# Performance work log

Hardware: AMD Instinct MI355X
Metric: run time of the kernel (lower is better)

Reference implementation:

```python
import jax, jax.numpy as jnp
import numpy as np

BN_EPS = 1e-3  # TF batch_norm default epsilon


def _three_nn(xyz1, xyz2):
    # xyz1: [B,N,3], xyz2: [B,M,3] -> squared dists [B,N,3], idx [B,N,3]
    d = (jnp.sum(xyz1 * xyz1, -1)[:, :, None]
         - 2.0 * jnp.einsum('bnd,bmd->bnm', xyz1, xyz2)
         + jnp.sum(xyz2 * xyz2, -1)[:, None, :])  # [B,N,M]
    neg, idx = jax.lax.top_k(-d, 3)
    return -neg, idx


def _conv_bn(x, W, b, g, beta, act):
    # 1x1 conv == dense over channel dim; BN over batch+point axes (B,N)
    y = jnp.einsum('bnc,cd->bnd', x, W) + b
    mu = jnp.mean(y, axis=(0, 1))
    var = jnp.var(y, axis=(0, 1))
    y = (y - mu) * jax.lax.rsqrt(var + BN_EPS) * g + beta
    return jax.nn.relu(y) if act else y


def setup_inputs() -> dict:
    key = jax.random.key(0)
    ks = jax.random.split(key, 6)
    B, N, M, C1, C2 = 16, 4096, 1024, 128, 256
    xyz1 = jax.random.normal(ks[0], (B, N, 3), jnp.float32)
    xyz2 = jax.random.normal(ks[1], (B, M, 3), jnp.float32)
    points1 = jax.random.normal(ks[2], (B, N, C1), jnp.float32)
    points2 = jax.random.normal(ks[3], (B, M, C2), jnp.float32)
    Cin = C1 + C2
    W0 = jax.random.normal(ks[4], (Cin, 256), jnp.float32) * (1.0 / np.sqrt(Cin))
    W1 = jax.random.normal(ks[5], (256, 128), jnp.float32) * (1.0 / np.sqrt(256))
    return {
        'xyz1': xyz1, 'points1': points1, 'xyz2': xyz2, 'points2': points2,
        'W0': W0, 'b0': jnp.zeros((256,), jnp.float32),
        'g0': jnp.ones((256,), jnp.float32), 'be0': jnp.zeros((256,), jnp.float32),
        'W1': W1, 'b1': jnp.zeros((128,), jnp.float32),
        'g1': jnp.ones((128,), jnp.float32), 'be1': jnp.zeros((128,), jnp.float32),
    }


def reference(xyz1, points1, xyz2, points2, W0, b0, g0, be0, W1, b1, g1, be1):
    dist, idx = _three_nn(xyz1, xyz2)            # [B,N,3]
    dist = jnp.maximum(dist, 1e-10)
    w = 1.0 / dist
    w = w / jnp.sum(w, axis=2, keepdims=True)    # [B,N,3]
    B = points2.shape[0]
    bidx = jnp.arange(B)[:, None, None]
    nbr = points2[bidx, idx]                     # [B,N,3,C2] gather
    interp = jnp.einsum('bnk,bnkc->bnc', w, nbr)
    x = jnp.concatenate([interp, points1], axis=2)  # [B,N,C1+C2]
    x = _conv_bn(x, W0, b0, g0, be0, act=True)
    x = _conv_bn(x, W1, b1, g1, be1, act=True)   # last_mlp_activation=True
    return x
```

## Files before the change

### kernel.cpp

```cpp
#include <hip/hip_runtime.h>
#include <hip/hip_bf16.h>
#include <stdint.h>

typedef __attribute__((ext_vector_type(4))) float f32x4;
typedef __attribute__((ext_vector_type(2))) float f32x2;
typedef __attribute__((ext_vector_type(8))) __bf16 bf16x8;

__device__ __forceinline__ unsigned short f2bf(float f) {
  unsigned u = __float_as_uint(f);
  unsigned r = (u + 0x7fffu + ((u >> 16) & 1u)) >> 16;
  return (unsigned short)r;
}
__device__ __forceinline__ float bf2f(unsigned short h) {
  return __uint_as_float(((unsigned)h) << 16);
}

__device__ __forceinline__ void load_lds16(const void* g, void* l) {
  __builtin_amdgcn_global_load_lds(
      (const __attribute__((address_space(1))) unsigned int*)g,
      (__attribute__((address_space(3))) unsigned int*)l, 16, 0, 0);
}

__device__ __forceinline__ void vwait(int n) {
  switch (n) {
    case 8: asm volatile("s_waitcnt vmcnt(8)" ::: "memory"); break;
    case 6: asm volatile("s_waitcnt vmcnt(6)" ::: "memory"); break;
    case 4: asm volatile("s_waitcnt vmcnt(4)" ::: "memory"); break;
    case 3: asm volatile("s_waitcnt vmcnt(3)" ::: "memory"); break;
    default: asm volatile("s_waitcnt vmcnt(0)" ::: "memory"); break;
  }
  __builtin_amdgcn_sched_barrier(0);
}

__global__ __launch_bounds__(256) void prep_kernel(
    const float* __restrict__ W0, const float* __restrict__ W1,
    const float* __restrict__ P2f, unsigned short* __restrict__ W0t,
    unsigned short* __restrict__ W1t, unsigned short* __restrict__ P2,
    float* __restrict__ stats) {
  int id = blockIdx.x * 256 + threadIdx.x;
  if (blockIdx.x == 0) {
    for (int i = threadIdx.x; i < 1536; i += 256) stats[i] = 0.f;
  }
  if (id < 256 * 384) {
    int n = id / 384, k = id - n * 384;
    W0t[id] = f2bf(W0[k * 256 + n]);
  }
  if (id < 128 * 256) {
    int n = id / 256, k = id - n * 256;
    W1t[id] = f2bf(W1[k * 128 + n]);
  }
  if (id < 1048576) {
    f32x4 v = ((const f32x4*)P2f)[id];
    ushort4 o = make_ushort4(f2bf(v[0]), f2bf(v[1]), f2bf(v[2]), f2bf(v[3]));
    ((ushort4*)P2)[id] = o;
  }
}

__global__ __launch_bounds__(256) void three_nn_kernel(
    const float* __restrict__ xyz1, const float* __restrict__ xyz2,
    float* __restrict__ W3, int* __restrict__ I3) {
  __shared__ __align__(16) float sx[1024];
  __shared__ __align__(16) float sy[1024];
  __shared__ __align__(16) float sz[1024];
  __shared__ __align__(16) float sn[1024];
  const int b = blockIdx.y;
  const int n0 = blockIdx.x * 32;
  const int tid = threadIdx.x;

  const float* xb = xyz2 + (size_t)b * 3072;
  for (int i = tid; i < 1024; i += 256) {
    float x = xb[i * 3 + 0], y = xb[i * 3 + 1], z = xb[i * 3 + 2];
    sx[i] = x; sy[i] = y; sz[i] = z;
    sn[i] = x * x + y * y + z * z;
  }
  __syncthreads();

  const int pt = tid >> 3, q = tid & 7;
  const int n = n0 + pt;
  const float* p = xyz1 + ((size_t)b * 4096 + n) * 3;
  const float px = p[0], py = p[1], pz = p[2];
  const float cx = -2.f * px, cy = -2.f * py, cz = -2.f * pz;

  float d0 = 3e38f, d1 = 3e38f, d2 = 3e38f;
  int i0 = 0, i1 = 0, i2 = 0;
  auto ins = [&](float e, int j) {
    const bool c0 = e < d0, c1 = e < d1, c2 = e < d2;
    const float nd2 = c1 ? d1 : (c2 ? e : d2);
    const int   ni2 = c1 ? i1 : (c2 ? j : i2);
    const float nd1 = c0 ? d0 : (c1 ? e : d1);
    const int   ni1 = c0 ? i0 : (c1 ? j : i1);
    d0 = c0 ? e : d0; i0 = c0 ? j : i0;
    d1 = nd1; i1 = ni1;
    d2 = nd2; i2 = ni2;
  };

  const f32x4* vx = (const f32x4*)sx;
  const f32x4* vy = (const f32x4*)sy;
  const f32x4* vz = (const f32x4*)sz;
  const f32x4* vn = (const f32x4*)sn;
  for (int jj = 0; jj < 32; jj++) {
    const int c = jj * 8 + q;
    f32x4 ax = vx[c], ay = vy[c], az = vz[c], an = vn[c];
#pragma unroll
    for (int u = 0; u < 4; u++) {
      float d = fmaf(ax[u], cx, fmaf(ay[u], cy, fmaf(az[u], cz, an[u])));
      ins(d, c * 4 + u);
    }
  }
#pragma unroll
  for (int off = 1; off <= 4; off <<= 1) {
    float e0 = __shfl_xor(d0, off, 64);
    float e1 = __shfl_xor(d1, off, 64);
    float e2 = __shfl_xor(d2, off, 64);
    int j0 = __shfl_xor(i0, off, 64);
    int j1 = __shfl_xor(i1, off, 64);
    int j2 = __shfl_xor(i2, off, 64);
    ins(e0, j0); ins(e1, j1); ins(e2, j2);
  }

  if (q == 0) {
    const float pn = fmaf(px, px, fmaf(py, py, pz * pz));
    float t0 = fmaxf(d0 + pn, 1e-10f);
    float t1 = fmaxf(d1 + pn, 1e-10f);
    float t2 = fmaxf(d2 + pn, 1e-10f);
    float w0 = 1.f / t0, w1 = 1.f / t1, w2 = 1.f / t2;
    float inv = 1.f / (w0 + w1 + w2);
    const int row = b * 4096 + n;
    W3[row * 3 + 0] = w0 * inv;
    W3[row * 3 + 1] = w1 * inv;
    W3[row * 3 + 2] = w2 * inv;
    I3[row * 3 + 0] = (b << 10) + i0;
    I3[row * 3 + 1] = (b << 10) + i1;
    I3[row * 3 + 2] = (b << 10) + i2;
  }
}

__global__ __launch_bounds__(256) void interp_concat_kernel(
    const float* __restrict__ points1, const unsigned short* __restrict__ P2,
    const float* __restrict__ W3, const int* __restrict__ I3,
    unsigned short* __restrict__ X) {
  const int gw = blockIdx.x * 4 + (threadIdx.x >> 6);
  const int lane = threadIdx.x & 63;
#pragma unroll 2
  for (int pp = 0; pp < 8; pp++) {
    const int row = gw * 8 + pp;
    const float w0 = W3[row * 3 + 0], w1 = W3[row * 3 + 1], w2 = W3[row * 3 + 2];
    const int g0 = I3[row * 3 + 0], g1 = I3[row * 3 + 1], g2 = I3[row * 3 + 2];
    const ushort4 a0 = *(const ushort4*)(P2 + (size_t)g0 * 256 + lane * 4);
    const ushort4 a1 = *(const ushort4*)(P2 + (size_t)g1 * 256 + lane * 4);
    const ushort4 a2 = *(const ushort4*)(P2 + (size_t)g2 * 256 + lane * 4);
    float o0 = bf2f(a0.x) * w0 + bf2f(a1.x) * w1 + bf2f(a2.x) * w2;
    float o1 = bf2f(a0.y) * w0 + bf2f(a1.y) * w1 + bf2f(a2.y) * w2;
    float o2 = bf2f(a0.z) * w0 + bf2f(a1.z) * w1 + bf2f(a2.z) * w2;
    float o3 = bf2f(a0.w) * w0 + bf2f(a1.w) * w1 + bf2f(a2.w) * w2;
    unsigned int lo = (unsigned)f2bf(o0) | ((unsigned)f2bf(o1) << 16);
    unsigned int hi = (unsigned)f2bf(o2) | ((unsigned)f2bf(o3) << 16);
    *(uint2*)(X + (size_t)row * 384 + lane * 4) = make_uint2(lo, hi);
    const f32x2 qv = ((const f32x2*)(points1 + (size_t)row * 128))[lane];
    unsigned int pq = (unsigned)f2bf(qv.x) | ((unsigned)f2bf(qv.y) << 16);
    *(unsigned int*)(X + (size_t)row * 384 + 256 + lane * 2) = pq;
  }
}

__global__ __launch_bounds__(512) void gemm1_kernel(
    const unsigned short* __restrict__ A, const unsigned short* __restrict__ Bt,
    const float* __restrict__ bvec, unsigned short* __restrict__ Y,
    float* __restrict__ ssum, float* __restrict__ ssq) {
  __shared__ __align__(16) char smem[131072];
  unsigned short* S = (unsigned short*)smem;
  const int m0 = blockIdx.x * 256;
  const int tid = threadIdx.x;
  const int wv = tid >> 6, lane = tid & 63;
  const int wm = wv >> 2, wn = wv & 3;
  f32x4 acc[8][4] = {};

  auto stage = [&](int t) {
    const int k0 = t * 32;
    unsigned short* Ab = S + (t & 3) * 16384;
    unsigned short* Bb = Ab + 8192;
#pragma unroll
    for (int i = 0; i < 2; i++) {
      const int c = (wv * 2 + i) * 64 + lane;
      const int row = c >> 2, kp = c & 3;
      const int gk = (kp ^ (row & 3)) * 8;
      load_lds16(A + (size_t)(m0 + row) * 384 + k0 + gk, Ab + (wv * 2 + i) * 512);
      load_lds16(Bt + (size_t)row * 384 + k0 + gk, Bb + (wv * 2 + i) * 512);
    }
  };

  stage(0); stage(1); stage(2);
  for (int t = 0; t < 12; ++t) {
    const int w = 11 - t;
    vwait(w >= 2 ? 8 : w * 4);
    __builtin_amdgcn_s_barrier();
    __builtin_amdgcn_sched_barrier(0);
    if (t < 9) stage(t + 3);
    const unsigned short* Ab = S + (t & 3) * 16384;
    const unsigned short* Bb = Ab + 8192;
    const int q = lane >> 4;
    bf16x8 af[8], bfr[4];
#pragma unroll
    for (int mf = 0; mf < 8; mf++) {
      const int r = wm * 128 + mf * 16 + (lane & 15);
      af[mf] = *(const bf16x8*)(Ab + r * 32 + (q ^ (r & 3)) * 8);
    }
#pragma unroll
    for (int nf = 0; nf < 4; nf++) {
      const int c = wn * 64 + nf * 16 + (lane & 15);
      bfr[nf] = *(const bf16x8*)(Bb + c * 32 + (q ^ (c & 3)) * 8);
    }
    __builtin_amdgcn_s_setprio(1);
#pragma unroll
    for (int mf = 0; mf < 8; mf++)
#pragma unroll
      for (int nf = 0; nf < 4; nf++)
        acc[mf][nf] = __builtin_amdgcn_mfma_f32_16x16x32_bf16(
            af[mf], bfr[nf], acc[mf][nf], 0, 0, 0);
    __builtin_amdgcn_s_setprio(0);
  }
  __syncthreads();

  float s[4] = {0, 0, 0, 0}, s2[4] = {0, 0, 0, 0};
  unsigned short* ep = S + wv * 8192;
#pragma unroll
  for (int mf = 0; mf < 8; mf++) {
#pragma unroll
    for (int nf = 0; nf < 4; nf++) {
      const float bv = bvec[wn * 64 + nf * 16 + (lane & 15)];
      f32x4 v = acc[mf][nf];
#pragma unroll
      for (int r = 0; r < 4; r++) {
        float y = v[r] + bv;
        s[nf] += y;
        s2[nf] += y * y;
        ep[(mf * 16 + (lane >> 4) * 4 + r) * 64 + nf * 16 + (lane & 15)] =
            f2bf(y);
      }
    }
  }
#pragma unroll
  for (int it = 0; it < 16; it++) {
    const int rr = it * 8 + (lane >> 3);
    *(uint4*)(Y + (size_t)(m0 + wm * 128 + rr) * 256 + wn * 64 + (lane & 7) * 8) =
        *(const uint4*)(ep + rr * 64 + (lane & 7) * 8);
  }

#pragma unroll
  for (int nf = 0; nf < 4; nf++) {
    s[nf] += __shfl_xor(s[nf], 16, 64);
    s[nf] += __shfl_xor(s[nf], 32, 64);
    s2[nf] += __shfl_xor(s2[nf], 16, 64);
    s2[nf] += __shfl_xor(s2[nf], 32, 64);
  }
  if (lane < 16) {
#pragma unroll
    for (int nf = 0; nf < 4; nf++) {
      const int col = wn * 64 + nf * 16 + lane;
      atomicAdd(&ssum[col], s[nf]);
      atomicAdd(&ssq[col], s2[nf]);
    }
  }
}

__device__ __forceinline__ uint4 bnpack8(bf16x8 r, f32x4 s0, f32x4 s1,
                                         f32x4 c0, f32x4 c1) {
  unsigned short o[8];
#pragma unroll
  for (int j = 0; j < 8; j++) {
    const float sj = j < 4 ? s0[j] : s1[j - 4];
    const float cj = j < 4 ? c0[j] : c1[j - 4];
    o[j] = f2bf(fmaxf(0.f, fmaf((float)r[j], sj, cj)));
  }
  return make_uint4((unsigned)o[0] | ((unsigned)o[1] << 16),
                    (unsigned)o[2] | ((unsigned)o[3] << 16),
                    (unsigned)o[4] | ((unsigned)o[5] << 16),
                    (unsigned)o[6] | ((unsigned)o[7] << 16));
}

__global__ __launch_bounds__(512) void gemm2_kernel(
    const unsigned short* __restrict__ Yin, const unsigned short* __restrict__ Bt,
    const float* __restrict__ sum1, const float* __restrict__ sq1,
    const float* __restrict__ g0, const float* __restrict__ be0,
    const float* __restrict__ bvec, unsigned short* __restrict__ Y2,
    float* __restrict__ ssum, float* __restrict__ ssq) {
  __shared__ __align__(16) char smem[100352];
  unsigned short* S = (unsigned short*)smem;
  float* scL = (float*)(smem + 98304);
  float* biL = scL + 256;
  const int m0 = blockIdx.x * 256;
  const int tid = threadIdx.x;
  const int wv = tid >> 6, lane = tid & 63;
  const int wm = wv >> 2, wn = wv & 3;
  f32x4 acc[8][2] = {};

  if (tid < 256) {
    const float invN = 1.0f / 65536.0f;
    float mu = sum1[tid] * invN;
    float var = sq1[tid] * invN - mu * mu;
    float sc = g0[tid] * rsqrtf(var + 1e-3f);
    scL[tid] = sc;
    biL[tid] = be0[tid] - mu * sc;
  }
  __syncthreads();

  bf16x8 arg[3][2];
  auto stageT = [&](int t, bf16x8(&ar)[2]) {
    const int k0 = t * 32;
#pragma unroll
    for (int j = 0; j < 2; j++) {
      const int c = tid + j * 512;
      const int row = c >> 2, kp = c & 3;
      const int gk = (kp ^ (row & 3)) * 8;
      ar[j] = *(const bf16x8*)(Yin + (size_t)(m0 + row) * 256 + k0 + gk);
    }
    const int cb = wv * 64 + lane;
    const int rowb = cb >> 2, kpb = cb & 3;
    const int gkb = (kpb ^ (rowb & 3)) * 8;
    load_lds16(Bt + (size_t)rowb * 256 + k0 + gkb,
               S + (t & 3) * 12288 + 8192 + wv * 512);
  };

  stageT(0, arg[0]); stageT(1, arg[1]); stageT(2, arg[2]);
#pragma unroll
  for (int t = 0; t < 8; ++t) {
    const int w = 7 - t;
    vwait(w >= 2 ? 6 : w * 3);
    unsigned short* Ab = S + (t & 3) * 12288;
#pragma unroll
    for (int j = 0; j < 2; j++) {
      const int c = tid + j * 512;
      const int row = c >> 2, kp = c & 3;
      const int gk = (kp ^ (row & 3)) * 8;
      const int kch = t * 32 + gk;
      const f32x4 sA = *(const f32x4*)(scL + kch);
      const f32x4 sB = *(const f32x4*)(scL + kch + 4);
      const f32x4 cA = *(const f32x4*)(biL + kch);
      const f32x4 cB = *(const f32x4*)(biL + kch + 4);
      *(uint4*)(Ab + c * 8) = bnpack8(arg[t % 3][j], sA, sB, cA, cB);
    }
    asm volatile("s_waitcnt lgkmcnt(0)" ::: "memory");
    __builtin_amdgcn_sched_barrier(0);
    __builtin_amdgcn_s_barrier();
    __builtin_amdgcn_sched_barrier(0);
    if (t < 5) stageT(t + 3, arg[t % 3]);
    const unsigned short* Bb = S + (t & 3) * 12288 + 8192;
    const int q = lane >> 4;
    bf16x8 af[8], bfr[2];
#pragma unroll
    for (int mf = 0; mf < 8; mf++) {
      const int r = wm * 128 + mf * 16 + (lane & 15);
      af[mf] = *(const bf16x8*)(Ab + r * 32 + (q ^ (r & 3)) * 8);
    }
#pragma unroll
    for (int nf = 0; nf < 2; nf++) {
      const int c = wn * 32 + nf * 16 + (lane & 15);
      bfr[nf] = *(const bf16x8*)(Bb + c * 32 + (q ^ (c & 3)) * 8);
    }
    __builtin_amdgcn_s_setprio(1);
#pragma unroll
    for (int mf = 0; mf < 8; mf++)
#pragma unroll
      for (int nf = 0; nf < 2; nf++)
        acc[mf][nf] = __builtin_amdgcn_mfma_f32_16x16x32_bf16(
            af[mf], bfr[nf], acc[mf][nf], 0, 0, 0);
    __builtin_amdgcn_s_setprio(0);
  }
  __syncthreads();

  float s[2] = {0, 0}, s2[2] = {0, 0};
  unsigned short* ep = S + wv * 4096;
#pragma unroll
  for (int mf = 0; mf < 8; mf++) {
#pragma unroll
    for (int nf = 0; nf < 2; nf++) {
      const float bv = bvec[wn * 32 + nf * 16 + (lane & 15)];
      f32x4 v = acc[mf][nf];
#pragma unroll
      for (int r = 0; r < 4; r++) {
        float y = v[r] + bv;
        s[nf] += y;
        s2[nf] += y * y;
        ep[(mf * 16 + (lane >> 4) * 4 + r) * 32 + nf * 16 + (lane & 15)] =
            f2bf(y);
      }
    }
  }
#pragma unroll
  for (int it = 0; it < 8; it++) {
    const int rr = it * 16 + (lane >> 2);
    *(uint4*)(Y2 + (size_t)(m0 + wm * 128 + rr) * 128 + wn * 32 + (lane & 3) * 8) =
        *(const uint4*)(ep + rr * 32 + (lane & 3) * 8);
  }

#pragma unroll
  for (int nf = 0; nf < 2; nf++) {
    s[nf] += __shfl_xor(s[nf], 16, 64);
    s[nf] += __shfl_xor(s[nf], 32, 64);
    s2[nf] += __shfl_xor(s2[nf], 16, 64);
    s2[nf] += __shfl_xor(s2[nf], 32, 64);
  }
  if (lane < 16) {
#pragma unroll
    for (int nf = 0; nf < 2; nf++) {
      const int col = wn * 32 + nf * 16 + lane;
      atomicAdd(&ssum[col], s[nf]);
      atomicAdd(&ssq[col], s2[nf]);
    }
  }
}

__global__ __launch_bounds__(256) void bnrelu_out_kernel(
    const unsigned short* __restrict__ Y2, const float* __restrict__ ssum,
    const float* __restrict__ ssq, const float* __restrict__ g,
    const float* __restrict__ be, float* __restrict__ out) {
  __shared__ __align__(16) float scL[128];
  __shared__ __align__(16) float biL[128];
  const int tid = threadIdx.x;
  if (tid < 128) {
    const float invN = 1.0f / 65536.0f;
    float mu = ssum[tid] * invN;
    float var = ssq[tid] * invN - mu * mu;
    float sc = g[tid] * rsqrtf(var + 1e-3f);
    scL[tid] = sc;
    biL[tid] = be[tid] - mu * sc;
  }
  __syncthreads();

  const size_t i = ((size_t)blockIdx.x * 256 + tid) * 8;
  const int c0 = (int)(i & 127);
  uint4 v = *(const uint4*)(Y2 + i);
  const f32x4 sA = *(const f32x4*)(scL + c0);
  const f32x4 sB = *(const f32x4*)(scL + c0 + 4);
  const f32x4 bA = *(const f32x4*)(biL + c0);
  const f32x4 bB = *(const f32x4*)(biL + c0 + 4);
  unsigned int w[4] = {v.x, v.y, v.z, v.w};
  f32x4 o0, o1;
#pragma unroll
  for (int q = 0; q < 2; q++) {
    o0[q * 2 + 0] = fmaxf(0.f, fmaf(bf2f((unsigned short)(w[q] & 0xffff)), sA[q * 2 + 0], bA[q * 2 + 0]));
    o0[q * 2 + 1] = fmaxf(0.f, fmaf(bf2f((unsigned short)(w[q] >> 16)),   sA[q * 2 + 1], bA[q * 2 + 1]));
    o1[q * 2 + 0] = fmaxf(0.f, fmaf(bf2f((unsigned short)(w[q + 2] & 0xffff)), sB[q * 2 + 0], bB[q * 2 + 0]));
    o1[q * 2 + 1] = fmaxf(0.f, fmaf(bf2f((unsigned short)(w[q + 2] >> 16)),   sB[q * 2 + 1], bB[q * 2 + 1]));
  }
  *(f32x4*)(out + i) = o0;
  *(f32x4*)(out + i + 4) = o1;
}

extern "C" void kernel_launch(void* const* d_in, const int* in_sizes, int n_in,
                              void* d_out, int out_size, void* d_ws,
                              size_t ws_size, hipStream_t stream) {
  const float* xyz1 = (const float*)d_in[0];
  const float* points1 = (const float*)d_in[1];
  const float* xyz2 = (const float*)d_in[2];
  const float* points2 = (const float*)d_in[3];
  const float* W0 = (const float*)d_in[4];
  const float* b0 = (const float*)d_in[5];
  const float* g0 = (const float*)d_in[6];
  const float* be0 = (const float*)d_in[7];
  const float* W1 = (const float*)d_in[8];
  const float* b1 = (const float*)d_in[9];
  const float* g1 = (const float*)d_in[10];
  const float* be1 = (const float*)d_in[11];

  char* ws = (char*)d_ws;
  unsigned short* X = (unsigned short*)(ws);
  unsigned short* Y2 = (unsigned short*)(ws);
  unsigned short* Y = (unsigned short*)(ws + 50331648);
  unsigned short* P2 = (unsigned short*)(ws + 50331648);
  float* W3 = (float*)(ws + 50331648 + 8388608);
  int* I3 = (int*)(ws + 50331648 + 8388608 + 786432);
  unsigned short* W0t = (unsigned short*)(ws + 83886080);
  unsigned short* W1t = (unsigned short*)(ws + 84082688);
  float* stats = (float*)(ws + 84148224);
  float* sum1 = stats, *sq1 = stats + 256;
  float* sum2 = stats + 1024, *sq2 = stats + 1152;
  float* outF = (float*)d_out;

  prep_kernel<<<4096, 256, 0, stream>>>(W0, W1, points2, W0t, W1t, P2, stats);
  three_nn_kernel<<<dim3(128, 16), 256, 0, stream>>>(xyz1, xyz2, W3, I3);
  interp_concat_kernel<<<2048, 256, 0, stream>>>(points1, P2, W3, I3, X);
  gemm1_kernel<<<256, 512, 0, stream>>>(X, W0t, b0, Y, sum1, sq1);
  gemm2_kernel<<<256, 512, 0, stream>>>(Y, W1t, sum1, sq1, g0, be0, b1, Y2,
                                        sum2, sq2);
  bnrelu_out_kernel<<<4096, 256, 0, stream>>>(Y2, sum2, sq2, g1, be1, outF);
}
```

Measured before the change: 132.6 us.

## Merge prep into three-NN launch and double gemm1 block to 16 waves

Fuses the bf16 conversion/prep kernel into the three-NN kernel as extra blocks of one launch, removing a kernel launch and letting the memory-bound prep overlap with the compute-bound nearest-neighbour search. Gemm1 now uses 1024 threads per block (16 waves, each owning a 64x64 sub-tile) instead of 8 waves with 128x64 tiles. This halves per-wave accumulator registers and the per-thread staging loads, with adjusted vmcnt waits. The trade-off is less MFMA reuse per LDS fragment load and more waves contending at each barrier.

```diff
diff --git a/kernel.cpp b/kernel.cpp
--- a/kernel.cpp
+++ b/kernel.cpp
@@ -27,45 +27,49 @@
     case 6: asm volatile("s_waitcnt vmcnt(6)" ::: "memory"); break;
     case 4: asm volatile("s_waitcnt vmcnt(4)" ::: "memory"); break;
     case 3: asm volatile("s_waitcnt vmcnt(3)" ::: "memory"); break;
+    case 2: asm volatile("s_waitcnt vmcnt(2)" ::: "memory"); break;
     default: asm volatile("s_waitcnt vmcnt(0)" ::: "memory"); break;
   }
   __builtin_amdgcn_sched_barrier(0);
 }
 
-__global__ __launch_bounds__(256) void prep_kernel(
+__global__ __launch_bounds__(256) void nn_prep_kernel(
+    const float* __restrict__ xyz1, const float* __restrict__ xyz2,
     const float* __restrict__ W0, const float* __restrict__ W1,
-    const float* __restrict__ P2f, unsigned short* __restrict__ W0t,
+    const float* __restrict__ P2f, float* __restrict__ W3,
+    int* __restrict__ I3, unsigned short* __restrict__ W0t,
     unsigned short* __restrict__ W1t, unsigned short* __restrict__ P2,
     float* __restrict__ stats) {
-  int id = blockIdx.x * 256 + threadIdx.x;
-  if (blockIdx.x == 0) {
-    for (int i = threadIdx.x; i < 1536; i += 256) stats[i] = 0.f;
-  }
-  if (id < 256 * 384) {
-    int n = id / 384, k = id - n * 384;
-    W0t[id] = f2bf(W0[k * 256 + n]);
-  }
-  if (id < 128 * 256) {
-    int n = id / 256, k = id - n * 256;
-    W1t[id] = f2bf(W1[k * 128 + n]);
-  }
-  if (id < 1048576) {
-    f32x4 v = ((const f32x4*)P2f)[id];
-    ushort4 o = make_ushort4(f2bf(v[0]), f2bf(v[1]), f2bf(v[2]), f2bf(v[3]));
-    ((ushort4*)P2)[id] = o;
-  }
-}
-
-__global__ __launch_bounds__(256) void three_nn_kernel(
-    const float* __restrict__ xyz1, const float* __restrict__ xyz2,
-    float* __restrict__ W3, int* __restrict__ I3) {
+  const int bid = blockIdx.x;
+  const int tid = threadIdx.x;
+  if (bid >= 2048) {
+    const int pid = bid - 2048;
+    const int id = pid * 256 + tid;
+    if (pid == 0) {
+      for (int i = tid; i < 1536; i += 256) stats[i] = 0.f;
+    }
+    if (id < 256 * 384) {
+      int n = id / 384, k = id - n * 384;
+      W0t[id] = f2bf(W0[k * 256 + n]);
+    }
+    if (id < 128 * 256) {
+      int n = id / 256, k = id - n * 256;
+      W1t[id] = f2bf(W1[k * 128 + n]);
+    }
+    if (id < 1048576) {
+      f32x4 v = ((const f32x4*)P2f)[id];
+      ushort4 o = make_ushort4(f2bf(v[0]), f2bf(v[1]), f2bf(v[2]), f2bf(v[3]));
+      ((ushort4*)P2)[id] = o;
+    }
+    return;
+  }
+
   __shared__ __align__(16) float sx[1024];
   __shared__ __align__(16) float sy[1024];
   __shared__ __align__(16) float sz[1024];
   __shared__ __align__(16) float sn[1024];
-  const int b = blockIdx.y;
-  const int n0 = blockIdx.x * 32;
-  const int tid = threadIdx.x;
+  const int b = bid >> 7;
+  const int n0 = (bid & 127) * 32;
 
   const float* xb = xyz2 + (size_t)b * 3072;
   for (int i = tid; i < 1024; i += 256) {
@@ -162,7 +166,7 @@
   }
 }
 
-__global__ __launch_bounds__(512) void gemm1_kernel(
+__global__ __launch_bounds__(1024) void gemm1_kernel(
     const unsigned short* __restrict__ A, const unsigned short* __restrict__ Bt,
     const float* __restrict__ bvec, unsigned short* __restrict__ Y,
     float* __restrict__ ssum, float* __restrict__ ssq) {
@@ -172,36 +176,32 @@
   const int tid = threadIdx.x;
   const int wv = tid >> 6, lane = tid & 63;
   const int wm = wv >> 2, wn = wv & 3;
-  f32x4 acc[8][4] = {};
+  f32x4 acc[4][4] = {};
 
   auto stage = [&](int t) {
     const int k0 = t * 32;
     unsigned short* Ab = S + (t & 3) * 16384;
     unsigned short* Bb = Ab + 8192;
-#pragma unroll
-    for (int i = 0; i < 2; i++) {
-      const int c = (wv * 2 + i) * 64 + lane;
-      const int row = c >> 2, kp = c & 3;
-      const int gk = (kp ^ (row & 3)) * 8;
-      load_lds16(A + (size_t)(m0 + row) * 384 + k0 + gk, Ab + (wv * 2 + i) * 512);
-      load_lds16(Bt + (size_t)row * 384 + k0 + gk, Bb + (wv * 2 + i) * 512);
-    }
+    const int row = tid >> 2, kp = tid & 3;
+    const int gk = (kp ^ (row & 3)) * 8;
+    load_lds16(A + (size_t)(m0 + row) * 384 + k0 + gk, Ab + wv * 512);
+    load_lds16(Bt + (size_t)row * 384 + k0 + gk, Bb + wv * 512);
   };
 
   stage(0); stage(1); stage(2);
   for (int t = 0; t < 12; ++t) {
     const int w = 11 - t;
-    vwait(w >= 2 ? 8 : w * 4);
+    vwait(w >= 2 ? 4 : w * 2);
     __builtin_amdgcn_s_barrier();
     __builtin_amdgcn_sched_barrier(0);
     if (t < 9) stage(t + 3);
     const unsigned short* Ab = S + (t & 3) * 16384;
     const unsigned short* Bb = Ab + 8192;
     const int q = lane >> 4;
-    bf16x8 af[8], bfr[4];
-#pragma unroll
-    for (int mf = 0; mf < 8; mf++) {
-      const int r = wm * 128 + mf * 16 + (lane & 15);
+    bf16x8 af[4], bfr[4];
+#pragma unroll
+    for (int mf = 0; mf < 4; mf++) {
+      const int r = wm * 64 + mf * 16 + (lane & 15);
       af[mf] = *(const bf16x8*)(Ab + r * 32 + (q ^ (r & 3)) * 8);
     }
 #pragma unroll
@@ -211,7 +211,7 @@
     }
     __builtin_amdgcn_s_setprio(1);
 #pragma unroll
-    for (int mf = 0; mf < 8; mf++)
+    for (int mf = 0; mf < 4; mf++)
 #pragma unroll
       for (int nf = 0; nf < 4; nf++)
         acc[mf][nf] = __builtin_amdgcn_mfma_f32_16x16x32_bf16(
@@ -221,9 +221,9 @@
   __syncthreads();
 
   float s[4] = {0, 0, 0, 0}, s2[4] = {0, 0, 0, 0};
-  unsigned short* ep = S + wv * 8192;
-#pragma unroll
-  for (int mf = 0; mf < 8; mf++) {
+  unsigned short* ep = S + wv * 4096;
+#pragma unroll
+  for (int mf = 0; mf < 4; mf++) {
 #pragma unroll
     for (int nf = 0; nf < 4; nf++) {
       const float bv = bvec[wn * 64 + nf * 16 + (lane & 15)];
@@ -239,9 +239,9 @@
     }
   }
 #pragma unroll
-  for (int it = 0; it < 16; it++) {
+  for (int it = 0; it < 8; it++) {
     const int rr = it * 8 + (lane >> 3);
-    *(uint4*)(Y + (size_t)(m0 + wm * 128 + rr) * 256 + wn * 64 + (lane & 7) * 8) =
+    *(uint4*)(Y + (size_t)(m0 + wm * 64 + rr) * 256 + wn * 64 + (lane & 7) * 8) =
         *(const uint4*)(ep + rr * 64 + (lane & 7) * 8);
   }
 
@@ -476,10 +476,10 @@
   float* sum2 = stats + 1024, *sq2 = stats + 1152;
   float* outF = (float*)d_out;
 
-  prep_kernel<<<4096, 256, 0, stream>>>(W0, W1, points2, W0t, W1t, P2, stats);
-  three_nn_kernel<<<dim3(128, 16), 256, 0, stream>>>(xyz1, xyz2, W3, I3);
+  nn_prep_kernel<<<6144, 256, 0, stream>>>(xyz1, xyz2, W0, W1, points2, W3, I3,
+                                           W0t, W1t, P2, stats);
   interp_concat_kernel<<<2048, 256, 0, stream>>>(points1, P2, W3, I3, X);
-  gemm1_kernel<<<256, 512, 0, stream>>>(X, W0t, b0, Y, sum1, sq1);
+  gemm1_kernel<<<256, 1024, 0, stream>>>(X, W0t, b0, Y, sum1, sq1);
   gemm2_kernel<<<256, 512, 0, stream>>>(Y, W1t, sum1, sq1, g0, be0, b1, Y2,
                                         sum2, sq2);
   bnrelu_out_kernel<<<4096, 256, 0, stream>>>(Y2, sum2, sq2, g1, be1, outF);
```

Measured after the change: 141.9 us. +7.0%, slower.
